# Kernel tuning notes

Measured on AMD Instinct MI355X. Metric: run time of the kernel, lower is better.

The kernel has to match this reference:

```python
import jax, jax.numpy as jnp
import numpy as np

N_DELTA, N_THETA, N_GAMMA = 64, 128, 512
N_TOTAL = N_DELTA + N_THETA + N_GAMMA  # 704
N_CLASSES = 1000
N_STEPS = 5
DT = 0.01
COUPLING = 2.0      # coupling_strength
PAC_DT = 0.3        # delta->theta phase-amplitude coupling depth
PAC_TG = 0.3        # theta->gamma phase-amplitude coupling depth
SPARSITY = 0.1      # PhaseToRateConverter sparsity (fraction of active units)
SHARP = 10.0        # softness of the 'soft' sparsification gate
TWO_PI = 2.0 * np.pi
B = 65536


def setup_inputs() -> dict:
    key = jax.random.key(0)
    k1, k2, k3, k4 = jax.random.split(key, 4)
    x = jax.random.normal(k1, (B, N_TOTAL), dtype=jnp.float32)
    # per-sample random initial phases in [0,1), scaled to [0,2pi) inside reference
    phase0 = jax.random.uniform(k2, (B, N_TOTAL), dtype=jnp.float32)
    W = jax.random.normal(k3, (N_CLASSES, N_TOTAL), dtype=jnp.float32) * 0.02
    b = jax.random.normal(k4, (N_CLASSES,), dtype=jnp.float32) * 0.02
    return {"x": x, "phase0": phase0, "W": W, "b": b}


def _kuramoto(phi):
    # mean-field within-band Kuramoto coupling: K * mean_j sin(phi_j - phi_i)
    S = jnp.mean(jnp.sin(phi), axis=-1, keepdims=True)
    C = jnp.mean(jnp.cos(phi), axis=-1, keepdims=True)
    return COUPLING * (S * jnp.cos(phi) - C * jnp.sin(phi))


def _mean_phase(phi):
    # circular mean phase of a band, shape (B,1)
    return jnp.arctan2(jnp.mean(jnp.sin(phi), axis=-1, keepdims=True),
                       jnp.mean(jnp.cos(phi), axis=-1, keepdims=True))


def _forward(x, phase0, W, b):
    freqs = jnp.concatenate([
        jnp.linspace(1.0, 4.0, N_DELTA),    # delta band Hz
        jnp.linspace(4.0, 8.0, N_THETA),    # theta band Hz
        jnp.linspace(30.0, 80.0, N_GAMMA),  # gamma band Hz
    ]).astype(x.dtype)
    phi = phase0 * TWO_PI                       # (B, N_TOTAL)
    amp = 1.0 + jnp.abs(x) * 0.01               # amplitude seeded by |x|*0.01 on unit base
    d = slice(0, N_DELTA)
    t = slice(N_DELTA, N_DELTA + N_THETA)
    g = slice(N_DELTA + N_THETA, N_TOTAL)

    def step(carry, _):
        phi, amp = carry
        dphi = TWO_PI * freqs + jnp.concatenate(
            [_kuramoto(phi[:, d]), _kuramoto(phi[:, t]), _kuramoto(phi[:, g])], axis=-1)
        psi_d = _mean_phase(phi[:, d])
        psi_t = _mean_phase(phi[:, t])
        # PAC: theta amplitude driven by delta phase, gamma amplitude by theta phase
        damp = jnp.concatenate([
            jnp.zeros_like(amp[:, d]),
            PAC_DT * amp[:, t] * jnp.cos(psi_d),
            PAC_TG * amp[:, g] * jnp.cos(psi_t),
        ], axis=-1)
        phi_new = jnp.mod(phi + DT * dphi, TWO_PI)
        amp_new = amp + DT * damp
        return (phi_new, amp_new), None

    (phi, amp), _ = jax.lax.scan(step, (phi, amp), None, length=N_STEPS)

    # PhaseToRateConverter, mode='soft': raw rate then soft top-(sparsity) gate
    raw = amp * 0.5 * (1.0 + jnp.cos(phi))                              # (B, N_TOTAL)
    thr = jnp.quantile(raw, 1.0 - SPARSITY, axis=-1, keepdims=True)    # per-sample threshold
    rate = raw * jax.nn.sigmoid((raw - thr) * SHARP)
    return rate @ W.T + b                                               # (B, N_CLASSES)


def reference(x, phase0, W, b):
    return _forward(x, phase0, W, b)
```

## Files before the change

### kernel.cpp

```cpp
#include <hip/hip_runtime.h>

#define NB 65536
#define NTOT 704
#define NCLS 1000
#define NPAD 1024
#define KDIM 704

typedef __attribute__((ext_vector_type(8))) short bf16x8;
typedef __attribute__((ext_vector_type(4))) float f32x4;
typedef __attribute__((ext_vector_type(2))) float f32x2;

#define WB_ELEMS (NPAD * KDIM)
#define LUT_DC_OFF (2u * (WB_ELEMS + 46137344u))
#define LUT_DS_OFF (LUT_DC_OFF + NTOT * 4u)

__device__ __forceinline__ f32x2 sp(float x) { return (f32x2){x, x}; }

template <int CTRL>
__device__ __forceinline__ float dpp_shuf(float v) {
  return __int_as_float(__builtin_amdgcn_update_dpp(0, __float_as_int(v), CTRL, 0xF, 0xF, true));
}
__device__ __forceinline__ float swz16(float v) {
  return __int_as_float(__builtin_amdgcn_ds_swizzle(__float_as_int(v), 0x401F));
}
__device__ __forceinline__ float wsum_f(float v) {
  v += dpp_shuf<0xB1>(v);
  v += dpp_shuf<0x4E>(v);
  v += dpp_shuf<0x141>(v);
  v += dpp_shuf<0x140>(v);
  v += swz16(v);
  v += __shfl_xor(v, 32, 64);
  return v;
}
__device__ __forceinline__ float wmax_f(float v) {
  v = fmaxf(v, dpp_shuf<0xB1>(v));
  v = fmaxf(v, dpp_shuf<0x4E>(v));
  v = fmaxf(v, dpp_shuf<0x141>(v));
  v = fmaxf(v, dpp_shuf<0x140>(v));
  v = fmaxf(v, swz16(v));
  v = fmaxf(v, __shfl_xor(v, 32, 64));
  return v;
}
__device__ __forceinline__ float wmin_f(float v) {
  v = fminf(v, dpp_shuf<0xB1>(v));
  v = fminf(v, dpp_shuf<0x4E>(v));
  v = fminf(v, dpp_shuf<0x141>(v));
  v = fminf(v, dpp_shuf<0x140>(v));
  v = fminf(v, swz16(v));
  v = fminf(v, __shfl_xor(v, 32, 64));
  return v;
}

__device__ __forceinline__ unsigned short f2bf(float v) {
  unsigned u = __float_as_uint(v);
  u = (u + 0x7FFFu + ((u >> 16) & 1u)) >> 16;
  return (unsigned short)u;
}

__global__ __launch_bounds__(256) void convw_kernel(const float* __restrict__ W,
                                                    unsigned short* __restrict__ Wb,
                                                    float* __restrict__ dcL,
                                                    float* __restrict__ dsL) {
  int i = blockIdx.x * 256 + threadIdx.x;
  if (i < NTOT) {
    float f;
    if (i < 64)       f = 1.0f + 3.0f * (float)i * (1.0f / 63.0f);
    else if (i < 192) f = 4.0f + 4.0f * (float)(i - 64) * (1.0f / 127.0f);
    else              f = 30.0f + 50.0f * (float)(i - 192) * (1.0f / 511.0f);
    const float rev = 0.01f * f;
    dcL[i] = __builtin_amdgcn_cosf(rev);
    dsL[i] = __builtin_amdgcn_sinf(rev);
  }
  if (i >= NPAD * KDIM) return;
  int n = i / KDIM;
  float v = (n < NCLS) ? W[i] : 0.0f;
  Wb[i] = f2bf(v);
}

__global__ __launch_bounds__(256) void sim_kernel(const float* __restrict__ x,
                                                  const float* __restrict__ p0,
                                                  const float* __restrict__ dcL,
                                                  const float* __restrict__ dsL,
                                                  unsigned short* __restrict__ rateb) {
  const int wave = threadIdx.x >> 6;
  const int lane = threadIdx.x & 63;
  const int sample = blockIdx.x * 4 + wave;
  const size_t base = (size_t)sample * NTOT;

  float sD, cD, ampD, dcD, dsD;
  f32x2 sPp[5], cPp[5], dc2[5], ds2[5], amp2[5];
  {
    const float p = p0[base + lane];
    sD = __builtin_amdgcn_sinf(p);
    cD = __builtin_amdgcn_cosf(p);
    ampD = fmaf(fabsf(x[base + lane]), 0.01f, 1.0f);
    dcD = dcL[lane]; dsD = dsL[lane];
  }
#pragma unroll
  for (int pr = 0; pr < 5; ++pr) {
    const int i0 = (1 + 2 * pr) * 64 + lane;
    const int i1 = i0 + 64;
    const float pa = p0[base + i0], pb = p0[base + i1];
    sPp[pr] = (f32x2){__builtin_amdgcn_sinf(pa), __builtin_amdgcn_sinf(pb)};
    cPp[pr] = (f32x2){__builtin_amdgcn_cosf(pa), __builtin_amdgcn_cosf(pb)};
    amp2[pr] = (f32x2){fmaf(fabsf(x[base + i0]), 0.01f, 1.0f),
                       fmaf(fabsf(x[base + i1]), 0.01f, 1.0f)};
    dc2[pr] = (f32x2){dcL[i0], dcL[i1]};
    ds2[pr] = (f32x2){dsL[i0], dsL[i1]};
  }

  float prodT = 1.0f, prodG = 1.0f;

#pragma unroll
  for (int st = 0; st < 5; ++st) {
    const float Sd = wsum_f(sD);
    const float Cd = wsum_f(cD);
    const float St = wsum_f(sPp[0].x + sPp[0].y);
    const float Ct = wsum_f(cPp[0].x + cPp[0].y);
    const f32x2 gs = (sPp[1] + sPp[2]) + (sPp[3] + sPp[4]);
    const f32x2 gc = (cPp[1] + cPp[2]) + (cPp[3] + cPp[4]);
    const float Sg = wsum_f(gs.x + gs.y);
    const float Cg = wsum_f(gc.x + gc.y);
    const float cpd = Cd * __builtin_amdgcn_rsqf(fmaf(Sd, Sd, Cd * Cd));
    const float cpt = Ct * __builtin_amdgcn_rsqf(fmaf(St, St, Ct * Ct));
    prodT *= fmaf(0.003f, cpd, 1.0f);
    prodG *= fmaf(0.003f, cpt, 1.0f);
    const float sdm = Sd * (0.02f / 64.0f),  cdm = Cd * (0.02f / 64.0f);
    const float stm = St * (0.02f / 128.0f), ctm = Ct * (0.02f / 128.0f);
    const float sgm = Sg * (0.02f / 512.0f), cgm = Cg * (0.02f / 512.0f);
    {
      const float eps = fmaf(-cdm, sD, sdm * cD);
      const float cd_ = fmaf(-dsD, eps, dcD);
      const float sd_ = fmaf(dcD, eps, dsD);
      const float sn = fmaf(cD, sd_, sD * cd_);
      const float cn = fmaf(-sD, sd_, cD * cd_);
      sD = sn; cD = cn;
    }
#pragma unroll
    for (int pr = 0; pr < 5; ++pr) {
      const f32x2 Sm = sp(pr == 0 ? stm : sgm);
      const f32x2 Cm = sp(pr == 0 ? ctm : cgm);
      const f32x2 s2 = sPp[pr], c2 = cPp[pr];
      const f32x2 eps = Sm * c2 - Cm * s2;
      const f32x2 cosd = dc2[pr] - ds2[pr] * eps;
      const f32x2 sind = ds2[pr] + dc2[pr] * eps;
      sPp[pr] = s2 * cosd + c2 * sind;
      cPp[pr] = c2 * cosd - s2 * sind;
    }
  }

  float raw[11];
  unsigned kk[11];
  {
    const float h = 0.5f * ampD;
    raw[0] = fmaf(h, cD, h);
  }
  const float hT = 0.5f * prodT, hG = 0.5f * prodG;
#pragma unroll
  for (int pr = 0; pr < 5; ++pr) {
    const f32x2 h2 = amp2[pr] * sp(pr == 0 ? hT : hG);
    const f32x2 r2 = h2 * cPp[pr] + h2;
    raw[1 + 2 * pr] = r2.x;
    raw[2 + 2 * pr] = r2.y;
  }
#pragma unroll
  for (int e = 0; e < 11; ++e) kk[e] = (unsigned)(raw[e] * 8192.0f);

  unsigned pre = 0;
#pragma unroll
  for (int bit = 13; bit >= 0; --bit) {
    const unsigned u = pre | ((1u << bit) - 1u);
    int cnt = 0;
#pragma unroll
    for (int e = 0; e < 11; ++e) cnt += (int)__popcll(__ballot(kk[e] <= u));
    if (cnt < 633) pre |= (1u << bit);
  }

  int clt = 0, ceq = 0;
#pragma unroll
  for (int e = 0; e < 11; ++e) {
    clt += (int)__popcll(__ballot(kk[e] < pre));
    ceq += (int)__popcll(__ballot(kk[e] == pre));
  }

  const float qv = 0.9f * 703.0f;
  float thr;
  if (clt + ceq >= 634) {
    thr = ((float)pre + 0.5f) * (1.0f / 8192.0f);
  } else {
    float mx = -1.0f, mn = 3.0e38f;
#pragma unroll
    for (int e = 0; e < 11; ++e) {
      mx = fmaxf(mx, (kk[e] == pre) ? raw[e] : -1.0f);
      mn = fminf(mn, (kk[e] > pre) ? raw[e] : 3.0e38f);
    }
    const float S632 = wmax_f(mx);
    const float S633 = wmin_f(mn);
    thr = S632 * (633.0f - qv) + S633 * (qv - 632.0f);
  }

#pragma unroll
  for (int e = 0; e < 11; ++e) {
    const float r = raw[e];
    const float t = __expf((thr - r) * 10.0f);
    const float sg = __builtin_amdgcn_rcpf(1.0f + t);
    rateb[base + e * 64 + lane] = f2bf(r * sg);
  }
}

#define BK3 64
#define NK3 (KDIM / BK3)

__device__ __forceinline__ void gload16(const unsigned short* g, unsigned short* l) {
  __builtin_amdgcn_global_load_lds((const __attribute__((address_space(1))) void*)g,
                                   (__attribute__((address_space(3))) void*)l,
                                   16, 0, 0);
}

__global__ __launch_bounds__(512, 2) void gemm_kernel(const unsigned short* __restrict__ A,
                                                      const unsigned short* __restrict__ Bw,
                                                      const float* __restrict__ bias,
                                                      float* __restrict__ C) {
  __shared__ __align__(16) unsigned short lsA[4 * 8192];
  __shared__ __align__(16) unsigned short lsB[4 * 8192];
  const int tid  = threadIdx.x;
  const int wave = tid >> 6;
  const int lane = tid & 63;

  const int bid = blockIdx.x;
  const int swz = (bid & 7) * 128 + (bid >> 3);
  const int bm = swz >> 2;
  const int bn = swz & 3;

  const int wr = wave >> 2;
  const int wc = wave & 3;

  f32x4 acc[8][4];
#pragma unroll
  for (int i = 0; i < 8; ++i)
#pragma unroll
    for (int j = 0; j < 4; ++j) acc[i][j] = (f32x4){0.f, 0.f, 0.f, 0.f};

  const int srow = tid >> 3;
  const int sc16 = ((tid & 7) ^ (srow & 7)) * 8;
  const unsigned short* Ab = A  + (size_t)(bm * 256) * KDIM;
  const unsigned short* Bb = Bw + (size_t)(bn * 256) * KDIM;

#define SHALF(dst, srcb, rb, k0)                                                      \
  gload16((srcb) + (size_t)((rb) + srow) * KDIM + (k0) + sc16, (dst) + tid * 8);      \
  gload16((srcb) + (size_t)((rb) + 64 + srow) * KDIM + (k0) + sc16, (dst) + 4096 + tid * 8);

  SHALF(lsA + 0 * 8192, Ab, 0, 0)
  SHALF(lsA + 1 * 8192, Ab, 128, 0)
  SHALF(lsB + 0 * 8192, Bb, 0, 0)
  SHALF(lsB + 1 * 8192, Bb, 128, 0)

  const int l15 = lane & 15;
  const int kq  = lane >> 4;

  bf16x8 af[4][2];
  bf16x8 bg[4][2];

#pragma unroll 1
  for (int t = 0; t < NK3; ++t) {
    const int d = t & 1, nd = d ^ 1;
    const int k0n = (t + 1) * BK3;
    const unsigned short* hA = lsA + (d * 2 + wr) * 8192;
    const unsigned short* hB = lsB + (d * 2 + (wc >> 1)) * 8192;
    const int rB0 = (wc & 1) * 64;

    if (t < NK3 - 1) {
      SHALF(lsA + (nd * 2 + 0) * 8192, Ab, 0, k0n)
      asm volatile("s_waitcnt vmcnt(2)" ::: "memory");
    } else {
      asm volatile("s_waitcnt vmcnt(0)" ::: "memory");
    }
    asm volatile("s_barrier" ::: "memory");
#pragma unroll
    for (int m = 0; m < 4; ++m) {
      const int lr = m * 16 + l15;
      af[m][0] = *(const bf16x8*)&hA[lr * 64 + ((kq ^ (lr & 7)) * 8)];
      af[m][1] = *(const bf16x8*)&hA[lr * 64 + (((kq + 4) ^ (lr & 7)) * 8)];
    }
#pragma unroll
    for (int n = 0; n < 2; ++n) {
      const int lr = rB0 + n * 16 + l15;
      bg[n][0] = *(const bf16x8*)&hB[lr * 64 + ((kq ^ (lr & 7)) * 8)];
      bg[n][1] = *(const bf16x8*)&hB[lr * 64 + (((kq + 4) ^ (lr & 7)) * 8)];
    }
    asm volatile("s_waitcnt lgkmcnt(0)" ::: "memory");
    __builtin_amdgcn_s_setprio(1);
#pragma unroll
    for (int m = 0; m < 4; ++m)
#pragma unroll
      for (int n = 0; n < 2; ++n) {
        acc[m][n] = __builtin_amdgcn_mfma_f32_16x16x32_bf16(af[m][0], bg[n][0], acc[m][n], 0, 0, 0);
        acc[m][n] = __builtin_amdgcn_mfma_f32_16x16x32_bf16(af[m][1], bg[n][1], acc[m][n], 0, 0, 0);
      }
    __builtin_amdgcn_s_setprio(0);
    asm volatile("s_barrier" ::: "memory");

#pragma unroll
    for (int n = 2; n < 4; ++n) {
      const int lr = rB0 + n * 16 + l15;
      bg[n][0] = *(const bf16x8*)&hB[lr * 64 + ((kq ^ (lr & 7)) * 8)];
      bg[n][1] = *(const bf16x8*)&hB[lr * 64 + (((kq + 4) ^ (lr & 7)) * 8)];
    }
    if (t < NK3 - 1) { SHALF(lsA + (nd * 2 + 1) * 8192, Ab, 128, k0n) }
    asm volatile("s_barrier" ::: "memory");
    asm volatile("s_waitcnt lgkmcnt(0)" ::: "memory");
    __builtin_amdgcn_s_setprio(1);
#pragma unroll
    for (int m = 0; m < 4; ++m)
#pragma unroll
      for (int n = 2; n < 4; ++n) {
        acc[m][n] = __builtin_amdgcn_mfma_f32_16x16x32_bf16(af[m][0], bg[n][0], acc[m][n], 0, 0, 0);
        acc[m][n] = __builtin_amdgcn_mfma_f32_16x16x32_bf16(af[m][1], bg[n][1], acc[m][n], 0, 0, 0);
      }
    __builtin_amdgcn_s_setprio(0);
    asm volatile("s_barrier" ::: "memory");

#pragma unroll
    for (int m = 0; m < 4; ++m) {
      const int lr = (m + 4) * 16 + l15;
      af[m][0] = *(const bf16x8*)&hA[lr * 64 + ((kq ^ (lr & 7)) * 8)];
      af[m][1] = *(const bf16x8*)&hA[lr * 64 + (((kq + 4) ^ (lr & 7)) * 8)];
    }
    if (t < NK3 - 1) { SHALF(lsB + (nd * 2 + 0) * 8192, Bb, 0, k0n) }
    asm volatile("s_barrier" ::: "memory");
    asm volatile("s_waitcnt lgkmcnt(0)" ::: "memory");
    __builtin_amdgcn_s_setprio(1);
#pragma unroll
    for (int m = 0; m < 4; ++m)
#pragma unroll
      for (int n = 0; n < 2; ++n) {
        acc[m + 4][n] = __builtin_amdgcn_mfma_f32_16x16x32_bf16(af[m][0], bg[n][0], acc[m + 4][n], 0, 0, 0);
        acc[m + 4][n] = __builtin_amdgcn_mfma_f32_16x16x32_bf16(af[m][1], bg[n][1], acc[m + 4][n], 0, 0, 0);
      }
    __builtin_amdgcn_s_setprio(0);
    asm volatile("s_barrier" ::: "memory");

    if (t < NK3 - 1) { SHALF(lsB + (nd * 2 + 1) * 8192, Bb, 128, k0n) }
    asm volatile("s_barrier" ::: "memory");
    __builtin_amdgcn_s_setprio(1);
#pragma unroll
    for (int m = 0; m < 4; ++m)
#pragma unroll
      for (int n = 2; n < 4; ++n) {
        acc[m + 4][n] = __builtin_amdgcn_mfma_f32_16x16x32_bf16(af[m][0], bg[n][0], acc[m + 4][n], 0, 0, 0);
        acc[m + 4][n] = __builtin_amdgcn_mfma_f32_16x16x32_bf16(af[m][1], bg[n][1], acc[m + 4][n], 0, 0, 0);
      }
    __builtin_amdgcn_s_setprio(0);
    asm volatile("s_barrier" ::: "memory");
  }

  const int crow0 = bm * 256 + wr * 128;
  const int ccol0 = bn * 256 + wc * 64;
  const int rql = (lane >> 4) * 4;
  const int cl  = lane & 15;
#pragma unroll
  for (int n = 0; n < 4; ++n) {
    const int col = ccol0 + n * 16 + cl;
    if (col < NCLS) {
      const float bb = bias[col];
#pragma unroll
      for (int m = 0; m < 8; ++m) {
#pragma unroll
        for (int r = 0; r < 4; ++r) {
          const int row = crow0 + m * 16 + rql + r;
          C[(size_t)row * NCLS + col] = acc[m][n][r] + bb;
        }
      }
    }
  }
}

extern "C" void kernel_launch(void* const* d_in, const int* in_sizes, int n_in,
                              void* d_out, int out_size, void* d_ws, size_t ws_size,
                              hipStream_t stream) {
  const float* x    = (const float*)d_in[0];
  const float* p0   = (const float*)d_in[1];
  const float* W    = (const float*)d_in[2];
  const float* bias = (const float*)d_in[3];
  float* out = (float*)d_out;

  unsigned short* Wb    = (unsigned short*)d_ws;
  unsigned short* rateb = (unsigned short*)d_ws + WB_ELEMS;
  float* dcL = (float*)((char*)d_ws + LUT_DC_OFF);
  float* dsL = (float*)((char*)d_ws + LUT_DS_OFF);

  convw_kernel<<<dim3((NPAD * KDIM + 255) / 256), dim3(256), 0, stream>>>(W, Wb, dcL, dsL);
  sim_kernel<<<dim3(NB / 4), dim3(256), 0, stream>>>(x, p0, dcL, dsL, rateb);
  gemm_kernel<<<dim3((NB / 256) * (NPAD / 256)), dim3(512), 0, stream>>>(rateb, Wb, bias, out);
}
```

Before: 324.0 us.

## Prefetch GEMM tiles two K-steps ahead and cut per-iteration barriers

The bf16 MFMA GEMM now issues global-to-LDS loads two K-steps ahead instead of one, preloading the first two stages in the prologue. Each stage is reloaded into the buffer that has just been consumed, right after a barrier confirms all waves have finished reading it. The iteration goes from about seven s_barriers to three, with sched_barrier fences keeping the instruction order. This should hide more global-load latency and cut synchronization stalls. The cost is a tighter buffer-reuse ordering that must stay correct, plus a vmcnt(8) wait that assumes a fixed number of outstanding loads.

```diff
diff --git a/kernel.cpp b/kernel.cpp
--- a/kernel.cpp
+++ b/kernel.cpp
@@ -211,6 +211,12 @@
 #define BK3 64
 #define NK3 (KDIM / BK3)
 
+#define FENCE __builtin_amdgcn_sched_barrier(0)
+#define BAR   do { FENCE; __builtin_amdgcn_s_barrier(); FENCE; } while (0)
+#define WVM8  do { asm volatile("s_waitcnt vmcnt(8)"); FENCE; } while (0)
+#define WVM0  do { asm volatile("s_waitcnt vmcnt(0)"); FENCE; } while (0)
+#define WLG0  do { asm volatile("s_waitcnt lgkmcnt(0)"); FENCE; } while (0)
+
 __device__ __forceinline__ void gload16(const unsigned short* g, unsigned short* l) {
   __builtin_amdgcn_global_load_lds((const __attribute__((address_space(1))) void*)g,
                                    (__attribute__((address_space(3))) void*)l,
@@ -254,6 +260,10 @@
   SHALF(lsA + 1 * 8192, Ab, 128, 0)
   SHALF(lsB + 0 * 8192, Bb, 0, 0)
   SHALF(lsB + 1 * 8192, Bb, 128, 0)
+  SHALF(lsA + 2 * 8192, Ab, 0, BK3)
+  SHALF(lsA + 3 * 8192, Ab, 128, BK3)
+  SHALF(lsB + 2 * 8192, Bb, 0, BK3)
+  SHALF(lsB + 3 * 8192, Bb, 128, BK3)
 
   const int l15 = lane & 15;
   const int kq  = lane >> 4;
@@ -263,19 +273,15 @@
 
 #pragma unroll 1
   for (int t = 0; t < NK3; ++t) {
-    const int d = t & 1, nd = d ^ 1;
-    const int k0n = (t + 1) * BK3;
+    const int d = t & 1;
+    const int k2 = (t + 2) * BK3;
+    const bool stg = (t + 2) < NK3;
     const unsigned short* hA = lsA + (d * 2 + wr) * 8192;
     const unsigned short* hB = lsB + (d * 2 + (wc >> 1)) * 8192;
     const int rB0 = (wc & 1) * 64;
 
-    if (t < NK3 - 1) {
-      SHALF(lsA + (nd * 2 + 0) * 8192, Ab, 0, k0n)
-      asm volatile("s_waitcnt vmcnt(2)" ::: "memory");
-    } else {
-      asm volatile("s_waitcnt vmcnt(0)" ::: "memory");
-    }
-    asm volatile("s_barrier" ::: "memory");
+    if (t == NK3 - 1) { WVM0; } else { WVM8; }
+    BAR;
 #pragma unroll
     for (int m = 0; m < 4; ++m) {
       const int lr = m * 16 + l15;
@@ -288,7 +294,7 @@
       bg[n][0] = *(const bf16x8*)&hB[lr * 64 + ((kq ^ (lr & 7)) * 8)];
       bg[n][1] = *(const bf16x8*)&hB[lr * 64 + (((kq + 4) ^ (lr & 7)) * 8)];
     }
-    asm volatile("s_waitcnt lgkmcnt(0)" ::: "memory");
+    WLG0;
     __builtin_amdgcn_s_setprio(1);
 #pragma unroll
     for (int m = 0; m < 4; ++m)
@@ -298,7 +304,7 @@
         acc[m][n] = __builtin_amdgcn_mfma_f32_16x16x32_bf16(af[m][1], bg[n][1], acc[m][n], 0, 0, 0);
       }
     __builtin_amdgcn_s_setprio(0);
-    asm volatile("s_barrier" ::: "memory");
+    FENCE;
 
 #pragma unroll
     for (int n = 2; n < 4; ++n) {
@@ -306,9 +312,13 @@
       bg[n][0] = *(const bf16x8*)&hB[lr * 64 + ((kq ^ (lr & 7)) * 8)];
       bg[n][1] = *(const bf16x8*)&hB[lr * 64 + (((kq + 4) ^ (lr & 7)) * 8)];
     }
-    if (t < NK3 - 1) { SHALF(lsA + (nd * 2 + 1) * 8192, Ab, 128, k0n) }
-    asm volatile("s_barrier" ::: "memory");
-    asm volatile("s_waitcnt lgkmcnt(0)" ::: "memory");
+    WLG0;
+    BAR;
+    if (stg) {
+      SHALF(lsB + (d * 2 + 0) * 8192, Bb, 0, k2)
+      SHALF(lsB + (d * 2 + 1) * 8192, Bb, 128, k2)
+    }
+    FENCE;
     __builtin_amdgcn_s_setprio(1);
 #pragma unroll
     for (int m = 0; m < 4; ++m)
@@ -318,7 +328,7 @@
         acc[m][n] = __builtin_amdgcn_mfma_f32_16x16x32_bf16(af[m][1], bg[n][1], acc[m][n], 0, 0, 0);
       }
     __builtin_amdgcn_s_setprio(0);
-    asm volatile("s_barrier" ::: "memory");
+    FENCE;
 
 #pragma unroll
     for (int m = 0; m < 4; ++m) {
@@ -326,9 +336,13 @@
       af[m][0] = *(const bf16x8*)&hA[lr * 64 + ((kq ^ (lr & 7)) * 8)];
       af[m][1] = *(const bf16x8*)&hA[lr * 64 + (((kq + 4) ^ (lr & 7)) * 8)];
     }
-    if (t < NK3 - 1) { SHALF(lsB + (nd * 2 + 0) * 8192, Bb, 0, k0n) }
-    asm volatile("s_barrier" ::: "memory");
-    asm volatile("s_waitcnt lgkmcnt(0)" ::: "memory");
+    WLG0;
+    BAR;
+    if (stg) {
+      SHALF(lsA + (d * 2 + 0) * 8192, Ab, 0, k2)
+      SHALF(lsA + (d * 2 + 1) * 8192, Ab, 128, k2)
+    }
+    FENCE;
     __builtin_amdgcn_s_setprio(1);
 #pragma unroll
     for (int m = 0; m < 4; ++m)
@@ -338,10 +352,8 @@
         acc[m + 4][n] = __builtin_amdgcn_mfma_f32_16x16x32_bf16(af[m][1], bg[n][1], acc[m + 4][n], 0, 0, 0);
       }
     __builtin_amdgcn_s_setprio(0);
-    asm volatile("s_barrier" ::: "memory");
-
-    if (t < NK3 - 1) { SHALF(lsB + (nd * 2 + 1) * 8192, Bb, 128, k0n) }
-    asm volatile("s_barrier" ::: "memory");
+    FENCE;
+
     __builtin_amdgcn_s_setprio(1);
 #pragma unroll
     for (int m = 0; m < 4; ++m)
@@ -351,7 +363,7 @@
         acc[m + 4][n] = __builtin_amdgcn_mfma_f32_16x16x32_bf16(af[m][1], bg[n][1], acc[m + 4][n], 0, 0, 0);
       }
     __builtin_amdgcn_s_setprio(0);
-    asm volatile("s_barrier" ::: "memory");
+    FENCE;
   }
 
   const int crow0 = bm * 256 + wr * 128;
```

Measured after the change: 295.9 us. 8.7% less time.
